# Kernel optimization log

Hardware: AMD Instinct MI355X
Metric: run time of the kernel (lower is better)

The kernel has to match this reference:

```python
import jax, jax.numpy as jnp
import numpy as np


def setup_inputs() -> dict:
    key = jax.random.key(0)
    k1, k2 = jax.random.split(key)
    B, S, HOP, L = 32, 524288, 256, 100
    frames = S // HOP
    # input hook asserts 0 <= phase <= 0.5
    wrapped_phase = jax.random.uniform(k1, (B, S), dtype=jnp.float32) * 0.5
    tables = jax.random.normal(k2, (B, frames + 1, L), dtype=jnp.float32)
    return {"wrapped_phase": wrapped_phase, "tables": tables, "hop_length": HOP}


def reference(wrapped_phase, tables, hop_length):
    # wrapped_phase: (B, S), hop_length divides S; tables: (B, S//hop + 1, L)
    B, S = wrapped_phase.shape
    frames = S // hop_length
    L = tables.shape[2]

    wp = wrapped_phase.reshape(B, frames, hop_length)          # (B, F, H)
    idx_raw = wp * L
    floor_idx = jnp.clip(idx_raw.astype(jnp.int32), 0, L - 1)  # (B, F, H)
    p = idx_raw - floor_idx.astype(wp.dtype)                   # frac along table axis

    # wrap-around pad of one sample along table axis: (B, F+1, L+1)
    padded = jnp.concatenate([tables, tables[:, :, :1]], axis=2)
    floor_flow = padded[:, :-1]                                # (B, F, L+1) frame t
    ceil_flow = padded[:, 1:]                                  # (B, F, L+1) frame t+1

    def lerp_table(flow):
        lo = jnp.take_along_axis(flow, floor_idx, axis=2)
        hi = jnp.take_along_axis(flow, floor_idx + 1, axis=2)
        return lo * (1 - p) + hi * p

    sel_floor = lerp_table(floor_flow)                         # (B, F, H)
    sel_ceil = lerp_table(ceil_flow)

    # interpolate across hop (frame) dimension
    p2 = jnp.arange(hop_length, dtype=wp.dtype) / hop_length   # (H,)
    final = sel_floor * (1 - p2) + sel_ceil * p2
    return final.reshape(B, -1)[:, :S]
```

## Files before the change

kernel.cpp:

```cpp
#include <hip/hip_runtime.h>

constexpr int HOP    = 256;
constexpr int L      = 100;
constexpr int FRAMES = 2048;
constexpr int B      = 32;
constexpr int FPB    = 16;
constexpr int GPB    = FRAMES / FPB;

__global__ __launch_bounds__(256) void glottal_kernel(
    const float* __restrict__ wp,
    const float* __restrict__ tables,
    float* __restrict__ out)
{
    __shared__ float2 pairs[FPB][L + 1];

    const int tid = threadIdx.x;
    const int b   = blockIdx.x >> 7;
    const int g   = blockIdx.x & (GPB - 1);
    const int f0  = g * FPB;

    const size_t blockbase = ((size_t)b * FRAMES + (size_t)f0) * HOP;

    float4 w[4];
#pragma unroll
    for (int j = 0; j < 4; ++j)
        w[j] = *reinterpret_cast<const float4*>(wp + blockbase + j * 1024 + tid * 4);

    const float* trow = tables + ((size_t)b * (FRAMES + 1) + (size_t)f0) * L;
    for (int i = tid; i < (FPB + 1) * (L + 1); i += 256) {
        int r  = i / (L + 1);
        int c  = i - r * (L + 1);
        int cs = (c == L) ? 0 : c;
        float v = trow[r * L + cs];
        if (r < FPB) pairs[r][c].x = v;
        if (r > 0)   pairs[r - 1][c].y = v;
    }
    __syncthreads();

    const int h0 = (tid & 63) * 4;
#pragma unroll
    for (int j = 0; j < 4; ++j) {
        const float2* row = pairs[j * 4 + (tid >> 6)];

        float wv[4] = {w[j].x, w[j].y, w[j].z, w[j].w};
        float res[4];
#pragma unroll
        for (int k = 0; k < 4; ++k) {
            float idx_raw = wv[k] * (float)L;
            int fi = (int)idx_raw;
            fi = fi < 0 ? 0 : (fi > L - 1 ? L - 1 : fi);
            float p  = idx_raw - (float)fi;
            float2 lo = row[fi];
            float2 hi = row[fi + 1];
            float sf = lo.x + (hi.x - lo.x) * p;
            float sc = lo.y + (hi.y - lo.y) * p;
            float p2 = (float)(h0 + k) * (1.0f / HOP);
            res[k] = sf + (sc - sf) * p2;
        }
        *reinterpret_cast<float4*>(out + blockbase + j * 1024 + tid * 4) =
            make_float4(res[0], res[1], res[2], res[3]);
    }
}

extern "C" void kernel_launch(void* const* d_in, const int* in_sizes, int n_in,
                              void* d_out, int out_size, void* d_ws, size_t ws_size,
                              hipStream_t stream) {
    const float* wp     = (const float*)d_in[0];
    const float* tables = (const float*)d_in[1];
    float* out = (float*)d_out;

    dim3 grid(B * GPB);
    glottal_kernel<<<grid, 256, 0, stream>>>(wp, tables, out);
}
```

Measured before the change: 140.2 us.

## Halve frames per block and store duplicated lo/hi table pairs for single LDS read

```diff
diff --git a/kernel.cpp b/kernel.cpp
--- a/kernel.cpp
+++ b/kernel.cpp
@@ -4,60 +4,77 @@
 constexpr int L      = 100;
 constexpr int FRAMES = 2048;
 constexpr int B      = 32;
-constexpr int FPB    = 16;
+constexpr int FPB    = 8;
 constexpr int GPB    = FRAMES / FPB;
+constexpr int NBLK   = B * GPB;
 
 __global__ __launch_bounds__(256) void glottal_kernel(
     const float* __restrict__ wp,
     const float* __restrict__ tables,
     float* __restrict__ out)
 {
-    __shared__ float2 pairs[FPB][L + 1];
+    __shared__ float2 Qp[FPB][2 * L];
 
     const int tid = threadIdx.x;
-    const int b   = blockIdx.x >> 7;
+    const int b   = blockIdx.x >> 8;
     const int g   = blockIdx.x & (GPB - 1);
     const int f0  = g * FPB;
 
     const size_t blockbase = ((size_t)b * FRAMES + (size_t)f0) * HOP;
 
-    float4 w[4];
+    const int wv   = tid >> 6;
+    const int lane = tid & 63;
+
+    float4 w0 = *reinterpret_cast<const float4*>(wp + blockbase + (2 * wv + 0) * HOP + lane * 4);
+    float4 w1 = *reinterpret_cast<const float4*>(wp + blockbase + (2 * wv + 1) * HOP + lane * 4);
+
+    {
+        const float* trow = tables + ((size_t)b * (FRAMES + 1) + (size_t)f0) * L;
+        const int r  = tid >> 5;
+        const int c0 = tid & 31;
 #pragma unroll
-    for (int j = 0; j < 4; ++j)
-        w[j] = *reinterpret_cast<const float4*>(wp + blockbase + j * 1024 + tid * 4);
-
-    const float* trow = tables + ((size_t)b * (FRAMES + 1) + (size_t)f0) * L;
-    for (int i = tid; i < (FPB + 1) * (L + 1); i += 256) {
-        int r  = i / (L + 1);
-        int c  = i - r * (L + 1);
-        int cs = (c == L) ? 0 : c;
-        float v = trow[r * L + cs];
-        if (r < FPB) pairs[r][c].x = v;
-        if (r > 0)   pairs[r - 1][c].y = v;
+        for (int k = 0; k < 4; ++k) {
+            const int c = c0 + 32 * k;
+            if (c <= L) {
+                const int cw = (c == L) ? 0 : c;
+                const float a  = trow[r * L + cw];
+                const float bb = trow[(r + 1) * L + cw];
+                if (c < L) Qp[r][2 * c]     = make_float2(a, bb);
+                if (c > 0) Qp[r][2 * c - 1] = make_float2(a, bb);
+            }
+        }
     }
     __syncthreads();
 
-    const int h0 = (tid & 63) * 4;
+    const float p2base = (float)(lane * 4) * (1.0f / HOP);
+
 #pragma unroll
-    for (int j = 0; j < 4; ++j) {
-        const float2* row = pairs[j * 4 + (tid >> 6)];
+    for (int j = 0; j < 2; ++j) {
+        const float2* row = Qp[2 * wv + j];
+        const float4  w   = j ? w1 : w0;
+        const float wv4[4] = {w.x, w.y, w.z, w.w};
 
-        float wv[4] = {w[j].x, w[j].y, w[j].z, w[j].w};
+        float4 q[4];
+        float  pf[4];
+#pragma unroll
+        for (int k = 0; k < 4; ++k) {
+            const float idx_raw = wv4[k] * (float)L;
+            int fi = (int)idx_raw;
+            fi = fi > L - 1 ? L - 1 : fi;
+            pf[k] = idx_raw - (float)fi;
+            q[k]  = *reinterpret_cast<const float4*>(&row[2 * fi]);
+        }
+
         float res[4];
 #pragma unroll
         for (int k = 0; k < 4; ++k) {
-            float idx_raw = wv[k] * (float)L;
-            int fi = (int)idx_raw;
-            fi = fi < 0 ? 0 : (fi > L - 1 ? L - 1 : fi);
-            float p  = idx_raw - (float)fi;
-            float2 lo = row[fi];
-            float2 hi = row[fi + 1];
-            float sf = lo.x + (hi.x - lo.x) * p;
-            float sc = lo.y + (hi.y - lo.y) * p;
-            float p2 = (float)(h0 + k) * (1.0f / HOP);
+            const float sf = q[k].x + (q[k].z - q[k].x) * pf[k];
+            const float sc = q[k].y + (q[k].w - q[k].y) * pf[k];
+            const float p2 = p2base + (float)k * (1.0f / HOP);
             res[k] = sf + (sc - sf) * p2;
         }
-        *reinterpret_cast<float4*>(out + blockbase + j * 1024 + tid * 4) =
+
+        *reinterpret_cast<float4*>(out + blockbase + (2 * wv + j) * HOP + lane * 4) =
             make_float4(res[0], res[1], res[2], res[3]);
     }
 }
@@ -69,6 +86,6 @@
     const float* tables = (const float*)d_in[1];
     float* out = (float*)d_out;
 
-    dim3 grid(B * GPB);
+    dim3 grid(NBLK);
     glottal_kernel<<<grid, 256, 0, stream>>>(wp, tables, out);
 }
```

After: 135.2 us. -3.6%, faster.
